# Kernel tuning notes

Measured on AMD Instinct MI355X. Metric: run time of the kernel, lower is better.

The kernel has to match this reference:

```python
import jax, jax.numpy as jnp
import numpy as np

D = 2048      # model_dim
H = 16        # num_heads
HD = D // H   # head_dim = 128
RQ = 512; RK = 512; RV = 512
B, T = 2, 2048


def setup_inputs() -> dict:
    key = jax.random.key(0)
    ks = jax.random.split(key, 9)
    s = lambda fan_in: 1.0 / np.sqrt(fan_in)
    return {
        "x":    jax.random.normal(ks[0], (B, T, D), dtype=jnp.float32),
        # nn.Linear weights stored [out, in]
        "wq_a": jax.random.uniform(ks[1], (RQ, D), jnp.float32, -s(D), s(D)),
        "wq_b": jax.random.uniform(ks[2], (H * HD, RQ), jnp.float32, -s(RQ), s(RQ)),
        "wk_a": jax.random.uniform(ks[3], (RK, D), jnp.float32, -s(D), s(D)),
        "wk_b": jax.random.uniform(ks[4], (H * HD, RK), jnp.float32, -s(RK), s(RK)),
        "wv_a": jax.random.uniform(ks[5], (RV, D), jnp.float32, -s(D), s(D)),
        "wv_b": jax.random.uniform(ks[6], (H * HD, RV), jnp.float32, -s(RV), s(RV)),
        "wo_w": jax.random.uniform(ks[7], (D, H * HD), jnp.float32, -s(H * HD), s(H * HD)),
        "wo_b": jax.random.uniform(ks[8], (D,), jnp.float32, -s(H * HD), s(H * HD)),
    }


def reference(x, wq_a, wq_b, wk_a, wk_b, wv_a, wv_b, wo_w, wo_b):
    b, t, d = x.shape
    # low-rank latent projections
    c_q = jnp.einsum('btd,rd->btr', x, wq_a)   # [b,t,RQ]
    c_k = jnp.einsum('btd,rd->btr', x, wk_a)   # [b,t,RK]
    c_v = jnp.einsum('btd,rd->btr', x, wv_a)   # [b,t,RV]
    # up-project and split heads: [b,h,t,hd]
    q = jnp.einsum('btr,er->bte', c_q, wq_b).reshape(b, t, H, HD).transpose(0, 2, 1, 3)
    k = jnp.einsum('btr,er->bte', c_k, wk_b).reshape(b, t, H, HD).transpose(0, 2, 1, 3)
    v = jnp.einsum('btr,er->bte', c_v, wv_b).reshape(b, t, H, HD).transpose(0, 2, 1, 3)
    # scaled dot-product attention (mask=None, dropout=0)
    scores = jnp.einsum('bhqd,bhkd->bhqk', q, k) / jnp.sqrt(jnp.float32(HD))
    attn = jax.nn.softmax(scores, axis=-1)
    out = jnp.einsum('bhqk,bhkd->bhqd', attn, v)
    out = out.transpose(0, 2, 1, 3).reshape(b, t, d)
    return jnp.einsum('bte,de->btd', out, wo_w) + wo_b
```

## Files before the change

kernel.cpp:

```cpp
#include <hip/hip_runtime.h>

typedef __attribute__((ext_vector_type(8))) short short8;
typedef __attribute__((ext_vector_type(4))) float f32x4;
typedef __attribute__((ext_vector_type(4))) float float4v;
typedef __attribute__((ext_vector_type(4))) unsigned short us4;

__device__ __forceinline__ unsigned short f2bf(float f) {
  union { float f; unsigned int u; } c; c.f = f;
  unsigned int u = c.u;
  u += 0x7fffu + ((u >> 16) & 1u);
  return (unsigned short)(u >> 16);
}

__device__ __forceinline__ unsigned int pkbf(float a, float b) {
  unsigned int r;
  asm("v_cvt_pk_bf16_f32 %0, %1, %2" : "=v"(r) : "v"(a), "v"(b));
  return r;
}

__device__ __forceinline__ float exp2r(float x) {
#if __has_builtin(__builtin_amdgcn_exp2f)
  return __builtin_amdgcn_exp2f(x);
#else
  return exp2f(x);
#endif
}

__device__ __forceinline__ void async16(const void* g, void* l) {
  __builtin_amdgcn_global_load_lds(
      (const __attribute__((address_space(1))) unsigned int*)g,
      (__attribute__((address_space(3))) unsigned int*)l, 16, 0, 0);
}

__device__ __forceinline__ f32x4 mfma16(short8 a, short8 b, f32x4 c) {
  return __builtin_amdgcn_mfma_f32_16x16x32_bf16(a, b, c, 0, 0, 0);
}

__global__ void cast_all(const float* __restrict__ x,
                         const float* __restrict__ wqa, const float* __restrict__ wqb,
                         const float* __restrict__ wka, const float* __restrict__ wkb,
                         const float* __restrict__ wva, const float* __restrict__ wvb,
                         const float* __restrict__ wow,
                         unsigned short* __restrict__ out) {
  int c = blockIdx.x * 256 + threadIdx.x;
  const int stride = gridDim.x * 256;
  for (; c < 4718592; c += stride) {
    int i = c << 2;
    const float* src; int off;
    if (i < 8388608)       { src = x;   off = 0; }
    else if (i < 9437184)  { src = wqa; off = 8388608; }
    else if (i < 10485760) { src = wka; off = 9437184; }
    else if (i < 11534336) { src = wva; off = 10485760; }
    else if (i < 12582912) { src = wqb; off = 11534336; }
    else if (i < 13631488) { src = wkb; off = 12582912; }
    else if (i < 14680064) { src = wvb; off = 13631488; }
    else                   { src = wow; off = 14680064; }
    float4v v = *(const float4v*)(src + (i - off));
    us4 r;
    r[0] = f2bf(v[0]); r[1] = f2bf(v[1]); r[2] = f2bf(v[2]); r[3] = f2bf(v[3]);
    *(us4*)(out + i) = r;
  }
}

template <int BN>
__device__ __forceinline__ void gemm_body(
    const unsigned short* __restrict__ A, int lda,
    const unsigned short* __restrict__ B, int ldb,
    void* __restrict__ Cv, int ldc,
    const float* __restrict__ bias, float qscale, int K, int mode) {
  constexpr int NT = BN / 32;
  __shared__ __align__(16) unsigned short As[128 * 64];
  __shared__ __align__(16) unsigned short Bs[BN * 64];
  const int tid  = threadIdx.x;
  const int wave = tid >> 6, lane = tid & 63;
  const int lr = lane & 15, lg = lane >> 4;
  const int lr7 = lr & 7;
  const int tile_m = blockIdx.y << 7;
  const int tile_n = blockIdx.x * BN;
  const int wm = (wave & 1) << 6;
  const int wn = (wave >> 1) * (BN / 2);

  f32x4 acc[4][NT];
#pragma unroll
  for (int i = 0; i < 4; i++)
#pragma unroll
    for (int j = 0; j < NT; j++) acc[i][j] = (f32x4)0.0f;

  const int srow = tid >> 3;
  const int cg = ((tid & 7) ^ (srow & 7)) << 3;
  const unsigned short* Ag = A + (size_t)(tile_m + srow) * lda + cg;
  const unsigned short* Bg = B + (size_t)(tile_n + srow) * ldb + cg;
  const size_t rowskipA = (size_t)32 * lda;
  const size_t rowskipB = (size_t)32 * ldb;
  unsigned short* AsW = As + wave * 512;
  unsigned short* BsW = Bs + wave * 512;

  for (int k0 = 0; k0 < K; k0 += 64) {
#pragma unroll
    for (int i = 0; i < 4; i++)
      async16(Ag + k0 + i * rowskipA, AsW + i * 2048);
#pragma unroll
    for (int i = 0; i < BN / 32; i++)
      async16(Bg + k0 + i * rowskipB, BsW + i * 2048);
    __syncthreads();
#pragma unroll
    for (int kk = 0; kk < 2; kk++) {
      short8 af[4], bf[NT];
#pragma unroll
      for (int mt = 0; mt < 4; mt++)
        af[mt] = *(const short8*)&As[(wm + mt * 16 + lr) * 64 + (((kk * 4 + lg) ^ lr7) << 3)];
#pragma unroll
      for (int nt = 0; nt < NT; nt++)
        bf[nt] = *(const short8*)&Bs[(wn + nt * 16 + lr) * 64 + (((kk * 4 + lg) ^ lr7) << 3)];
#pragma unroll
      for (int mt = 0; mt < 4; mt++)
#pragma unroll
        for (int nt = 0; nt < NT; nt++)
          acc[mt][nt] = mfma16(af[mt], bf[nt], acc[mt][nt]);
    }
    __syncthreads();
  }

#pragma unroll
  for (int mt = 0; mt < 4; mt++) {
#pragma unroll
    for (int nt = 0; nt < NT; nt++) {
#pragma unroll
      for (int r = 0; r < 4; r++) {
        int row = tile_m + wm + mt * 16 + lg * 4 + r;
        int col = tile_n + wn + nt * 16 + lr;
        float v = acc[mt][nt][r];
        if (mode == 0) {
          ((unsigned short*)Cv)[(size_t)row * ldc + col] = f2bf(v);
        } else if (mode == 3) {
          ((unsigned short*)Cv)[(size_t)row * ldc + col] = f2bf(v * qscale);
        } else if (mode == 1) {
          int tl = row & 2047;
          int key = tl & 63;
          int tp = (tl & ~63) | ((key & 15) << 2) | (key >> 4);
          ((unsigned short*)Cv)[((size_t)((row >> 11) << 11) + col) * 2048 + tp] = f2bf(v);
        } else {
          ((float*)Cv)[(size_t)row * ldc + col] = v + bias[col];
        }
      }
    }
  }
}

__global__ __launch_bounds__(256)
void gemm_k128(const unsigned short* __restrict__ A, int lda,
               const unsigned short* __restrict__ B, int ldb,
               void* __restrict__ C, int ldc, const float* __restrict__ bias,
               int K, int mode) {
  gemm_body<128>(A, lda, B, ldb, C, ldc, bias, 1.0f, K, mode);
}

__global__ __launch_bounds__(256)
void gemm_k64(const unsigned short* __restrict__ A, int lda,
              const unsigned short* __restrict__ B, int ldb,
              void* __restrict__ C, int ldc, const float* __restrict__ bias,
              int K, int mode) {
  gemm_body<64>(A, lda, B, ldb, C, ldc, bias, 1.0f, K, mode);
}

__global__ __launch_bounds__(256)
void gemm_up(const unsigned short* __restrict__ cdown,
             const unsigned short* __restrict__ wup,
             unsigned short* __restrict__ qb,
             unsigned short* __restrict__ kb,
             unsigned short* __restrict__ vtb) {
  const int z = blockIdx.z;
  const unsigned short* A = cdown + z * 512;
  const unsigned short* B = wup + (size_t)z * 1048576;
  void* C; int mode; float qs = 1.0f;
  if (z == 0)      { C = qb;  mode = 3; qs = 0.12751744f; }
  else if (z == 1) { C = kb;  mode = 0; }
  else             { C = vtb; mode = 1; }
  gemm_body<128>(A, 1536, B, 512, C, 2048, nullptr, qs, 512, mode);
}

__global__ __launch_bounds__(512)
void attn(const unsigned short* __restrict__ q,
          const unsigned short* __restrict__ k,
          const unsigned short* __restrict__ vt,
          unsigned short* __restrict__ o) {
  __shared__ __align__(16) unsigned short Ks[2][64 * 128];
  __shared__ __align__(16) unsigned short Vs[2][128 * 64];
  __shared__ __align__(16) unsigned short Ps[8][16 * 64];

  const int tid  = threadIdx.x;
  const int wave = tid >> 6, lane = tid & 63;
  const int lr = lane & 15, lg = lane >> 4;
  const int lin = blockIdx.x + (blockIdx.y << 4);
  const int xcd = lin & 7;
  const int lcl = lin >> 3;
  const int bh = (xcd << 2) | (lcl & 3);
  const int b = bh >> 4, h = bh & 15;
  const int q0 = (lcl >> 2) << 7;

  const size_t qrow = (size_t)(b * 2048 + q0 + wave * 16 + lr);
  short8 qf[4];
#pragma unroll
  for (int kk = 0; kk < 4; kk++)
    qf[kk] = *(const short8*)(q + qrow * 2048 + h * 128 + kk * 32 + lg * 8);

  f32x4 oacc[8];
  f32x4 lacc = (f32x4)0.0f;
#pragma unroll
  for (int n2 = 0; n2 < 8; n2++) oacc[n2] = (f32x4)0.0f;

  short8 ones;
#pragma unroll
  for (int j = 0; j < 8; j++) ones[j] = (short)0x3F80;

  const unsigned short* kg = k  + (size_t)(b * 2048 + (tid >> 4)) * 2048 + h * 128
                               + ((((tid & 15) ^ (tid >> 4)) & 15) << 3);
  const unsigned short* vg = vt + (size_t)(bh * 128 + (tid >> 3)) * 2048
                               + (((tid & 7) ^ ((tid >> 3) & 7)) << 3);
  const int lr7 = lr & 7;

#pragma unroll
  for (int i = 0; i < 2; i++) {
    async16(kg + (size_t)(i * 32) * 2048, &Ks[0][i * 4096 + wave * 512]);
    async16(vg + (size_t)(i * 64) * 2048, &Vs[0][i * 4096 + wave * 512]);
  }
  __syncthreads();

  for (int kt = 0; kt < 2048; kt += 64) {
    const int buf = (kt >> 6) & 1;
    if (kt < 2048 - 64) {
      const int nk = kt + 64;
#pragma unroll
      for (int i = 0; i < 2; i++) {
        async16(kg + (size_t)(nk + i * 32) * 2048, &Ks[buf ^ 1][i * 4096 + wave * 512]);
        async16(vg + nk + (size_t)(i * 64) * 2048, &Vs[buf ^ 1][i * 4096 + wave * 512]);
      }
    }
    const unsigned short* KsB = Ks[buf];
    const unsigned short* VsB = Vs[buf];

    f32x4 sv[4];
#pragma unroll
    for (int nt = 0; nt < 4; nt++) sv[nt] = (f32x4)0.0f;
    __builtin_amdgcn_s_setprio(1);
#pragma unroll
    for (int nt = 0; nt < 4; nt++) {
#pragma unroll
      for (int kk = 0; kk < 4; kk++) {
        short8 kf = *(const short8*)&KsB[(nt * 16 + lr) * 128 + (((kk * 4 + lg) ^ lr) << 3)];
        sv[nt] = mfma16(qf[kk], kf, sv[nt]);
      }
    }
    __builtin_amdgcn_s_setprio(0);

#pragma unroll
    for (int r = 0; r < 4; r++) {
      float p0 = exp2r(sv[0][r]);
      float p1 = exp2r(sv[1][r]);
      float p2 = exp2r(sv[2][r]);
      float p3 = exp2r(sv[3][r]);
      uint2 pk; pk.x = pkbf(p0, p1); pk.y = pkbf(p2, p3);
      int row = lg * 4 + r;
      *(uint2*)&Ps[wave][row * 64 + ((lr ^ (lg << 2)) << 2)] = pk;
    }

    __builtin_amdgcn_s_setprio(1);
#pragma unroll
    for (int kt2 = 0; kt2 < 2; kt2++) {
      short8 pf = *(const short8*)&Ps[wave]
          [lr * 64 + (((kt2 * 8 + lg * 2) ^ ((lr >> 2) << 2)) << 2)];
      lacc = mfma16(pf, ones, lacc);
#pragma unroll
      for (int n2 = 0; n2 < 8; n2++) {
        short8 vf = *(const short8*)&VsB[(n2 * 16 + lr) * 64 + (((kt2 * 4 + lg) ^ lr7) << 3)];
        oacc[n2] = mfma16(pf, vf, oacc[n2]);
      }
    }
    __builtin_amdgcn_s_setprio(0);

    __syncthreads();
  }

  f32x4 inv;
#pragma unroll
  for (int r = 0; r < 4; r++) inv[r] = 1.0f / lacc[r];
#pragma unroll
  for (int n2 = 0; n2 < 8; n2++)
#pragma unroll
    for (int r = 0; r < 4; r++) {
      size_t row = (size_t)(b * 2048 + q0 + wave * 16 + lg * 4 + r);
      o[row * 2048 + h * 128 + n2 * 16 + lr] = f2bf(oacc[n2][r] * inv[r]);
    }
}

extern "C" void kernel_launch(void* const* d_in, const int* in_sizes, int n_in,
                              void* d_out, int out_size, void* d_ws, size_t ws_size,
                              hipStream_t stream) {
  const float* x    = (const float*)d_in[0];
  const float* wq_a = (const float*)d_in[1];
  const float* wq_b = (const float*)d_in[2];
  const float* wk_a = (const float*)d_in[3];
  const float* wk_b = (const float*)d_in[4];
  const float* wv_a = (const float*)d_in[5];
  const float* wv_b = (const float*)d_in[6];
  const float* wo_w = (const float*)d_in[7];
  const float* wo_b = (const float*)d_in[8];
  float* out = (float*)d_out;

  unsigned short* ws = (unsigned short*)d_ws;
  unsigned short* xb    = ws;
  unsigned short* wdown = ws + 8388608;
  unsigned short* wupb  = ws + 11534336;
  unsigned short* wow   = ws + 14680064;
  unsigned short* cdown = ws + 18874368;
  unsigned short* qb    = ws + 25165824;
  unsigned short* kb    = ws + 33554432;
  unsigned short* vtb   = ws + 41943040;
  unsigned short* ao    = ws + 50331648;

  cast_all<<<dim3(2048), dim3(256), 0, stream>>>(x, wq_a, wq_b, wk_a, wk_b, wv_a, wv_b, wo_w, ws);

  gemm_k64<<<dim3(24, 32), dim3(256), 0, stream>>>(xb, 2048, wdown, 2048, cdown, 1536, nullptr, 2048, 0);

  gemm_up<<<dim3(16, 32, 3), dim3(256), 0, stream>>>(cdown, wupb, qb, kb, vtb);

  attn<<<dim3(16, 32), dim3(512), 0, stream>>>(qb, kb, vtb, ao);

  gemm_k64<<<dim3(32, 32), dim3(256), 0, stream>>>(ao, 2048, wow, 2048, out, 2048, wo_b, 2048, 2);
}
```

Baseline: 332.3 us.

## Software-pipeline attention loop: overlap next QK^T and softmax with current PV

Restructures the flash-attention inner loop so each iteration computes the QK^T scores for tile t+1 while doing the PV accumulation for tile t, with a prologue and an epilogue. K is prefetched two tiles ahead and V one tile ahead, and the buffer roles are staggered to match. The aim is to hide the exp/pack and LDS round-trip latency behind MFMA work and to let independent MFMA chains interleave. The cost is more live registers (P fragments held across iterations) and more complex buffer indexing.

```diff
diff --git a/kernel.cpp b/kernel.cpp
--- a/kernel.cpp
+++ b/kernel.cpp
@@ -223,36 +223,23 @@
   for (int i = 0; i < 2; i++) {
     async16(kg + (size_t)(i * 32) * 2048, &Ks[0][i * 4096 + wave * 512]);
     async16(vg + (size_t)(i * 64) * 2048, &Vs[0][i * 4096 + wave * 512]);
+    async16(kg + (size_t)(64 + i * 32) * 2048, &Ks[1][i * 4096 + wave * 512]);
   }
   __syncthreads();
 
-  for (int kt = 0; kt < 2048; kt += 64) {
-    const int buf = (kt >> 6) & 1;
-    if (kt < 2048 - 64) {
-      const int nk = kt + 64;
-#pragma unroll
-      for (int i = 0; i < 2; i++) {
-        async16(kg + (size_t)(nk + i * 32) * 2048, &Ks[buf ^ 1][i * 4096 + wave * 512]);
-        async16(vg + nk + (size_t)(i * 64) * 2048, &Vs[buf ^ 1][i * 4096 + wave * 512]);
-      }
-    }
-    const unsigned short* KsB = Ks[buf];
-    const unsigned short* VsB = Vs[buf];
-
+  short8 pfA, pfB;
+  {
     f32x4 sv[4];
 #pragma unroll
     for (int nt = 0; nt < 4; nt++) sv[nt] = (f32x4)0.0f;
-    __builtin_amdgcn_s_setprio(1);
 #pragma unroll
     for (int nt = 0; nt < 4; nt++) {
 #pragma unroll
       for (int kk = 0; kk < 4; kk++) {
-        short8 kf = *(const short8*)&KsB[(nt * 16 + lr) * 128 + (((kk * 4 + lg) ^ lr) << 3)];
+        short8 kf = *(const short8*)&Ks[0][(nt * 16 + lr) * 128 + (((kk * 4 + lg) ^ lr) << 3)];
         sv[nt] = mfma16(qf[kk], kf, sv[nt]);
       }
     }
-    __builtin_amdgcn_s_setprio(0);
-
 #pragma unroll
     for (int r = 0; r < 4; r++) {
       float p0 = exp2r(sv[0][r]);
@@ -263,22 +250,84 @@
       int row = lg * 4 + r;
       *(uint2*)&Ps[wave][row * 64 + ((lr ^ (lg << 2)) << 2)] = pk;
     }
+    pfA = *(const short8*)&Ps[wave][lr * 64 + (((lg * 2) ^ ((lr >> 2) << 2)) << 2)];
+    pfB = *(const short8*)&Ps[wave][lr * 64 + (((8 + lg * 2) ^ ((lr >> 2) << 2)) << 2)];
+  }
+  __syncthreads();
+
+  for (int t = 0; t < 31; ++t) {
+    const int buf = t & 1;
+    if (t < 30) {
+#pragma unroll
+      for (int i = 0; i < 2; i++)
+        async16(kg + (size_t)((t + 2) * 64 + i * 32) * 2048, &Ks[buf][i * 4096 + wave * 512]);
+    }
+#pragma unroll
+    for (int i = 0; i < 2; i++)
+      async16(vg + (t + 1) * 64 + (size_t)(i * 64) * 2048, &Vs[buf ^ 1][i * 4096 + wave * 512]);
+
+    const unsigned short* KsN = Ks[buf ^ 1];
+    const unsigned short* VsB = Vs[buf];
 
     __builtin_amdgcn_s_setprio(1);
-#pragma unroll
-    for (int kt2 = 0; kt2 < 2; kt2++) {
-      short8 pf = *(const short8*)&Ps[wave]
-          [lr * 64 + (((kt2 * 8 + lg * 2) ^ ((lr >> 2) << 2)) << 2)];
-      lacc = mfma16(pf, ones, lacc);
-#pragma unroll
-      for (int n2 = 0; n2 < 8; n2++) {
-        short8 vf = *(const short8*)&VsB[(n2 * 16 + lr) * 64 + (((kt2 * 4 + lg) ^ lr7) << 3)];
-        oacc[n2] = mfma16(pf, vf, oacc[n2]);
+    f32x4 sv[4];
+#pragma unroll
+    for (int nt = 0; nt < 4; nt++) sv[nt] = (f32x4)0.0f;
+#pragma unroll
+    for (int nt = 0; nt < 4; nt++) {
+#pragma unroll
+      for (int kk = 0; kk < 4; kk++) {
+        short8 kf = *(const short8*)&KsN[(nt * 16 + lr) * 128 + (((kk * 4 + lg) ^ lr) << 3)];
+        sv[nt] = mfma16(qf[kk], kf, sv[nt]);
       }
     }
+
+    lacc = mfma16(pfA, ones, lacc);
+#pragma unroll
+    for (int n2 = 0; n2 < 8; n2++) {
+      short8 vf = *(const short8*)&VsB[(n2 * 16 + lr) * 64 + ((lg ^ lr7) << 3)];
+      oacc[n2] = mfma16(pfA, vf, oacc[n2]);
+    }
+    lacc = mfma16(pfB, ones, lacc);
+#pragma unroll
+    for (int n2 = 0; n2 < 8; n2++) {
+      short8 vf = *(const short8*)&VsB[(n2 * 16 + lr) * 64 + (((4 + lg) ^ lr7) << 3)];
+      oacc[n2] = mfma16(pfB, vf, oacc[n2]);
+    }
     __builtin_amdgcn_s_setprio(0);
 
+#pragma unroll
+    for (int r = 0; r < 4; r++) {
+      float p0 = exp2r(sv[0][r]);
+      float p1 = exp2r(sv[1][r]);
+      float p2 = exp2r(sv[2][r]);
+      float p3 = exp2r(sv[3][r]);
+      uint2 pk; pk.x = pkbf(p0, p1); pk.y = pkbf(p2, p3);
+      int row = lg * 4 + r;
+      *(uint2*)&Ps[wave][row * 64 + ((lr ^ (lg << 2)) << 2)] = pk;
+    }
+    pfA = *(const short8*)&Ps[wave][lr * 64 + (((lg * 2) ^ ((lr >> 2) << 2)) << 2)];
+    pfB = *(const short8*)&Ps[wave][lr * 64 + (((8 + lg * 2) ^ ((lr >> 2) << 2)) << 2)];
+
     __syncthreads();
+  }
+
+  {
+    const unsigned short* VsB = Vs[1];
+    __builtin_amdgcn_s_setprio(1);
+    lacc = mfma16(pfA, ones, lacc);
+#pragma unroll
+    for (int n2 = 0; n2 < 8; n2++) {
+      short8 vf = *(const short8*)&VsB[(n2 * 16 + lr) * 64 + ((lg ^ lr7) << 3)];
+      oacc[n2] = mfma16(pfA, vf, oacc[n2]);
+    }
+    lacc = mfma16(pfB, ones, lacc);
+#pragma unroll
+    for (int n2 = 0; n2 < 8; n2++) {
+      short8 vf = *(const short8*)&VsB[(n2 * 16 + lr) * 64 + (((4 + lg) ^ lr7) << 3)];
+      oacc[n2] = mfma16(pfB, vf, oacc[n2]);
+    }
+    __builtin_amdgcn_s_setprio(0);
   }
 
   f32x4 inv;
```

After: 347.9 us. 4.7% more time.
